# Kernel optimization log

Measured on AMD Instinct MI355X. Metric: run time of the kernel, lower is better.

Reference implementation:

```python
import jax, jax.numpy as jnp
import numpy as np

K = 16  # num neighbors


def setup_inputs() -> dict:
    key = jax.random.key(0)
    ks = jax.random.split(key, 10)
    B, N, d_in, d_out = 4, 8192, 64, 128
    h = d_out // 2
    return {
        "xyz": jax.random.normal(ks[0], (B, 3, N), jnp.float32),
        "feature": jax.random.normal(ks[1], (B, d_in, N), jnp.float32),
        "w1": jax.random.normal(ks[2], (h, 10), jnp.float32) * 0.1,
        "b1": jax.random.normal(ks[3], (h,), jnp.float32) * 0.1,
        "w2": jax.random.normal(ks[4], (h, h), jnp.float32) * 0.1,
        "b2": jax.random.normal(ks[5], (h,), jnp.float32) * 0.1,
        "w3": jax.random.normal(ks[6], (h, h), jnp.float32) * 0.1,
        "b3": jax.random.normal(ks[7], (h,), jnp.float32) * 0.1,
        "ws": jax.random.normal(ks[8], (d_out, d_in), jnp.float32) * 0.1,
        "bs": jax.random.normal(ks[9], (d_out,), jnp.float32) * 0.1,
    }


def reference(xyz, feature, w1, b1, w2, b2, w3, b3, ws, bs):
    # xyz: [B,3,N], feature: [B,d_in,N]
    xyz_t = jnp.transpose(xyz, (0, 2, 1))  # [B,N,3]
    sq = jnp.sum(xyz_t * xyz_t, axis=-1)  # [B,N]
    # squared pairwise distance [B,N,N]
    dist = sq[:, :, None] + sq[:, None, :] - 2.0 * jnp.einsum("bnc,bmc->bnm", xyz_t, xyz_t)
    _, idx = jax.lax.top_k(-dist, K)  # smallest-k -> [B,N,K]
    # gather neighbor coords: [B,N,K,3]
    knn_xyz = jax.vmap(lambda pts, ind: pts[ind])(xyz_t, idx)
    center = jnp.broadcast_to(xyz_t[:, :, None, :], knn_xyz.shape)  # [B,N,K,3]
    diff = knn_xyz - center
    dsq = jnp.sum(diff * diff, axis=-1, keepdims=True)  # [B,N,K,1]
    pos = jnp.concatenate([center, knn_xyz, diff, dsq], axis=-1)  # [B,N,K,10]
    # three 1x1 convs over channel dim (no activations, faithful to source)
    h = jnp.einsum("bnkc,oc->bnko", pos, w1) + b1
    h = jnp.einsum("bnkc,oc->bnko", h, w2) + b2
    h = jnp.einsum("bnkc,oc->bnko", h, w3) + b3
    fe = jnp.max(h, axis=2)  # max-pool over neighbors -> [B,N,d_out//2]
    fe = jnp.transpose(fe, (0, 2, 1))  # [B,d_out//2,N]
    shortcut = jnp.einsum("bcn,oc->bon", feature, ws) + bs[None, :, None]
    return jnp.concatenate([fe, fe], axis=1) + shortcut  # [B,d_out,N]
```

## Files before the change

### kernel.cpp

```cpp
#include <hip/hip_runtime.h>

#define B_ 4
#define N_ 8192
#define DIN 64
#define HDIM 64
#define DOUT 128
#define KNN 16
#define QPB 64
#define PART 8
#define NTHR (QPB * PART)
#define CHUNK (N_ / PART)
#define CAP 16
#define BLOCKS_PER_B (N_ / QPB)

__global__ __launch_bounds__(256) void k_prep(
    const float* __restrict__ xyz,
    const float* __restrict__ w1, const float* __restrict__ b1,
    const float* __restrict__ w2, const float* __restrict__ b2,
    const float* __restrict__ w3, const float* __restrict__ b3,
    float4* __restrict__ pk, float4* __restrict__ prm) {
  const int blk = blockIdx.x, t = threadIdx.x;
  const int b = blk >> 5;
  const int m = ((blk & 31) << 8) + t;
  const float* xb = xyz + (size_t)b * 3 * N_;
  float x = xb[m], y = xb[N_ + m], z = xb[2 * N_ + m];
  float sq = __fadd_rn(__fadd_rn(__fmul_rn(x, x), __fmul_rn(y, y)), __fmul_rn(z, z));
  pk[((size_t)b << 13) + m] = make_float4(x, y, z, sq);

  if (blk == 0) {
    __shared__ float M2[HDIM][10];
    __shared__ float bb[HDIM];
    const int o = t;
    if (o < HDIM) {
      float r[10];
#pragma unroll
      for (int c = 0; c < 10; c++) r[c] = 0.f;
      float s = b2[o];
      for (int l = 0; l < HDIM; l++) {
        float w = w2[o * HDIM + l];
#pragma unroll
        for (int c = 0; c < 10; c++) r[c] = fmaf(w, w1[l * 10 + c], r[c]);
        s = fmaf(w, b1[l], s);
      }
#pragma unroll
      for (int c = 0; c < 10; c++) M2[o][c] = r[c];
      bb[o] = s;
    }
    __syncthreads();
    if (o < HDIM) {
      float r3[10];
#pragma unroll
      for (int c = 0; c < 10; c++) r3[c] = 0.f;
      float bc = b3[o];
      for (int l = 0; l < HDIM; l++) {
        float w = w3[o * HDIM + l];
#pragma unroll
        for (int c = 0; c < 10; c++) r3[c] = fmaf(w, M2[l][c], r3[c]);
        bc = fmaf(w, bb[l], bc);
      }
      prm[o]      = make_float4(r3[0] - r3[6], r3[1] - r3[7], r3[2] - r3[8], bc);
      prm[64 + o] = make_float4(r3[3] + r3[6], r3[4] + r3[7], r3[5] + r3[8], r3[9]);
    }
  }
}

#define INSERT16(VARR, IARR, VMAX, DVAL, MIDX)                    \
  {                                                               \
    bool done = false;                                            \
    _Pragma("unroll") for (int _i = 0; _i < KNN; _i++) {          \
      bool hit = (!done) && (VARR[_i] == VMAX);                   \
      if (hit) { VARR[_i] = (DVAL); IARR[_i] = (MIDX); }          \
      done = done | hit;                                          \
    }                                                             \
    float _a = fmaxf(fmaxf(fmaxf(VARR[0], VARR[1]), fmaxf(VARR[2], VARR[3])),   \
                     fmaxf(fmaxf(VARR[4], VARR[5]), fmaxf(VARR[6], VARR[7])));  \
    float _b = fmaxf(fmaxf(fmaxf(VARR[8], VARR[9]), fmaxf(VARR[10], VARR[11])), \
                     fmaxf(fmaxf(VARR[12], VARR[13]), fmaxf(VARR[14], VARR[15])));\
    VMAX = fmaxf(_a, _b);                                         \
  }

#define MAX16(VARR, VMAX)                                         \
  {                                                               \
    float _a = fmaxf(fmaxf(fmaxf(VARR[0], VARR[1]), fmaxf(VARR[2], VARR[3])),   \
                     fmaxf(fmaxf(VARR[4], VARR[5]), fmaxf(VARR[6], VARR[7])));  \
    float _b = fmaxf(fmaxf(fmaxf(VARR[8], VARR[9]), fmaxf(VARR[10], VARR[11])), \
                     fmaxf(fmaxf(VARR[12], VARR[13]), fmaxf(VARR[14], VARR[15])));\
    VMAX = fmaxf(_a, _b);                                         \
  }

#define FLUSH()                                                   \
  {                                                               \
    for (int c_ = 0; c_ < cnt; c_++) {                            \
      float fd_ = poolF[c_ * NTHR + t];                           \
      int fm_ = poolI[c_ * NTHR + t];                             \
      if (fd_ < vmax) { INSERT16(v, id, vmax, fd_, fm_); }        \
    }                                                             \
    cnt = 0;                                                      \
    atomicMin(&tau[q], __float_as_uint(vmax));                    \
    gate = fminf(vmax, __uint_as_float(tau[q]));                  \
  }

__global__ __launch_bounds__(512, 4) void k_knn_fe(
    const float4* __restrict__ pk, const float4* __restrict__ prm,
    float* __restrict__ feBuf) {
  const int blk = blockIdx.x;
  const int b  = blk / BLOCKS_PER_B;
  const int n0 = (blk % BLOCKS_PER_B) * QPB;
  const int t = threadIdx.x;
  const int q = t & 63;
  const int j = __builtin_amdgcn_readfirstlane(t >> 6);

  __shared__ unsigned tau[QPB];
  __shared__ float4 prmL[2 * HDIM];
  __shared__ float poolF[CAP * NTHR];
  __shared__ unsigned short poolI[CAP * NTHR];

  if (t < QPB) tau[t] = 0x7f800000u;
  for (int i = t; i < 2 * HDIM; i += NTHR) prmL[i] = prm[i];

  const float4 qv = pk[((size_t)b << 13) + n0 + q];
  const float qx = qv.x, qy = qv.y, qz = qv.z, qs = qv.w;

  const float INF = __uint_as_float(0x7f800000u);
  float v[KNN]; int id[KNN];
#pragma unroll
  for (int i = 0; i < KNN; i++) { v[i] = INF; id[i] = 0; }
  float vmax = INF, gate = INF;
  int cnt = 0;
  __syncthreads();

  const float4* pj = pk + ((size_t)b << 13) + j * CHUNK;
  for (int u0 = 0; u0 < CHUNK; u0 += 8) {
    if (__any(cnt > CAP - 8)) { FLUSH(); }
    gate = fminf(gate, __uint_as_float(tau[q]));
    float4 c[8];
#pragma unroll
    for (int e = 0; e < 8; e++) c[e] = pj[u0 + e];
#pragma unroll
    for (int e = 0; e < 8; e++) {
      float dot = fmaf(c[e].z, qz, fmaf(c[e].y, qy, __fmul_rn(c[e].x, qx)));
      float d = __fsub_rn(__fadd_rn(qs, c[e].w), __fmul_rn(2.0f, dot));
      if (d < gate) {
        poolF[cnt * NTHR + t] = d;
        poolI[cnt * NTHR + t] = (unsigned short)(j * CHUNK + u0 + e);
        cnt++;
      }
    }
  }
  FLUSH();
  __syncthreads();

#pragma unroll
  for (int i = 0; i < KNN; i++) {
    poolF[(j * KNN + i) * QPB + q] = v[i];
    poolI[(j * KNN + i) * QPB + q] = (unsigned short)id[i];
  }
  __syncthreads();

  float fv[KNN]; int fid[KNN]; float fm = INF;
  if (j < 4) {
    const int r0 = (2 * j) * KNN, r1 = (2 * j + 1) * KNN;
#pragma unroll
    for (int i = 0; i < KNN; i++) {
      fv[i] = poolF[(r0 + i) * QPB + q];
      fid[i] = poolI[(r0 + i) * QPB + q];
    }
    MAX16(fv, fm);
    for (int s = 0; s < KNN; s++) {
      float d = poolF[(r1 + s) * QPB + q];
      if (d < fm) { int m_ = poolI[(r1 + s) * QPB + q]; INSERT16(fv, fid, fm, d, m_); }
    }
#pragma unroll
    for (int i = 0; i < KNN; i++) {
      poolF[(r0 + i) * QPB + q] = fv[i];
      poolI[(r0 + i) * QPB + q] = (unsigned short)fid[i];
    }
  }
  __syncthreads();

  if (j == 0) {
    for (int g = 1; g < 4; g++) {
      const int rg = (2 * g) * KNN;
      for (int s = 0; s < KNN; s++) {
        float d = poolF[(rg + s) * QPB + q];
        if (d < fm) { int m_ = poolI[(rg + s) * QPB + q]; INSERT16(fv, fid, fm, d, m_); }
      }
    }
#pragma unroll
    for (int i = 0; i < KNN; i++) poolI[i * QPB + q] = (unsigned short)fid[i];
  }
  __syncthreads();

#pragma unroll
  for (int kk = 0; kk < 2; kk++) {
    int k = j * 2 + kk;
    int m = poolI[k * QPB + q];
    float4 c = pk[((size_t)b << 13) + m];
    float dx = __fsub_rn(c.x, qx), dy = __fsub_rn(c.y, qy), dz = __fsub_rn(c.z, qz);
    float dsq = __fadd_rn(__fadd_rn(__fmul_rn(dx, dx), __fmul_rn(dy, dy)),
                          __fmul_rn(dz, dz));
    poolF[k * QPB + q] = c.x;
    poolF[(KNN + k) * QPB + q] = c.y;
    poolF[(2 * KNN + k) * QPB + q] = c.z;
    poolF[(3 * KNN + k) * QPB + q] = dsq;
  }
  __syncthreads();

  float nx[KNN], ny[KNN], nz[KNN], nd[KNN];
#pragma unroll
  for (int k = 0; k < KNN; k++) {
    nx[k] = poolF[k * QPB + q];
    ny[k] = poolF[(KNN + k) * QPB + q];
    nz[k] = poolF[(2 * KNN + k) * QPB + q];
    nd[k] = poolF[(3 * KNN + k) * QPB + q];
  }
  float fo[8];
#pragma unroll
  for (int oi = 0; oi < 8; oi++) {
    int o = j * 8 + oi;
    float4 pA = prmL[o], pB = prmL[HDIM + o];
    float basev = fmaf(qz, pA.z, fmaf(qy, pA.y, fmaf(qx, pA.x, pA.w)));
    float mx = -INF;
#pragma unroll
    for (int k = 0; k < KNN; k++) {
      float tv = fmaf(nz[k], pB.z,
                 fmaf(ny[k], pB.y,
                 fmaf(nx[k], pB.x, __fmul_rn(nd[k], pB.w))));
      mx = fmaxf(mx, tv);
    }
    fo[oi] = basev + mx;
  }
  float* feRow = feBuf + (size_t)(b * N_ + n0 + q) * HDIM + j * 8;
  ((float4*)feRow)[0] = make_float4(fo[0], fo[1], fo[2], fo[3]);
  ((float4*)feRow)[1] = make_float4(fo[4], fo[5], fo[6], fo[7]);
}

__global__ __launch_bounds__(256) void k_out(
    const float* __restrict__ feature, const float* __restrict__ wsM,
    const float* __restrict__ bs, const float* __restrict__ feBuf,
    float* __restrict__ out) {
  const int blk = blockIdx.x;
  const int b  = blk / BLOCKS_PER_B;
  const int n0 = (blk % BLOCKS_PER_B) * QPB;
  const int t = threadIdx.x;
  const int q = t & 63;
  const int jj = t >> 6;
  __shared__ float featL[DIN][QPB];
  __shared__ float wsL[DOUT][DIN];
#pragma unroll
  for (int r = 0; r < DIN; r += 4) {
    int c = r + jj;
    featL[c][q] = feature[(size_t)(b * DIN + c) * N_ + n0 + q];
  }
  for (int i = t; i < DOUT * DIN; i += 256) ((float*)wsL)[i] = wsM[i];
  __syncthreads();
  float f[DIN];
#pragma unroll
  for (int c = 0; c < DIN; c++) f[c] = featL[c][q];
  const float* feRow = feBuf + (size_t)(b * N_ + n0 + q) * HDIM;
  const int o0 = jj * 32;
  for (int oi = 0; oi < 32; oi++) {
    int o = o0 + oi;
    const float4* wr = (const float4*)wsL[o];
    float acc = 0.f;
#pragma unroll
    for (int c4 = 0; c4 < DIN / 4; c4++) {
      float4 w = wr[c4];
      acc = fmaf(w.x, f[4 * c4], acc);
      acc = fmaf(w.y, f[4 * c4 + 1], acc);
      acc = fmaf(w.z, f[4 * c4 + 2], acc);
      acc = fmaf(w.w, f[4 * c4 + 3], acc);
    }
    float r = acc + bs[o] + feRow[o & 63];
    out[(size_t)(b * DOUT + o) * N_ + n0 + q] = r;
  }
}

extern "C" void kernel_launch(void* const* d_in, const int* in_sizes, int n_in,
                              void* d_out, int out_size, void* d_ws, size_t ws_size,
                              hipStream_t stream) {
  const float* xyz     = (const float*)d_in[0];
  const float* feature = (const float*)d_in[1];
  const float* w1 = (const float*)d_in[2];
  const float* b1 = (const float*)d_in[3];
  const float* w2 = (const float*)d_in[4];
  const float* b2 = (const float*)d_in[5];
  const float* w3 = (const float*)d_in[6];
  const float* b3 = (const float*)d_in[7];
  const float* wsM = (const float*)d_in[8];
  const float* bs  = (const float*)d_in[9];
  float* out = (float*)d_out;

  float4* prm  = (float4*)d_ws;
  float4* pkB  = (float4*)((char*)d_ws + 8192);
  float* feBuf = (float*)((char*)d_ws + 8192 + (size_t)B_ * N_ * 16);

  hipLaunchKernelGGL(k_prep, dim3(128), dim3(256), 0, stream,
                     xyz, w1, b1, w2, b2, w3, b3, pkB, prm);
  hipLaunchKernelGGL(k_knn_fe, dim3(B_ * BLOCKS_PER_B), dim3(NTHR), 0, stream,
                     pkB, prm, feBuf);
  hipLaunchKernelGGL(k_out, dim3(B_ * BLOCKS_PER_B), dim3(256), 0, stream,
                     feature, wsM, bs, feBuf, out);
}
```

Measured before the change: 301.6 us.

## Fuse shortcut conv into KNN kernel, seed top-k from first points, tree-merge partials

Folds the output kernel (shortcut 1x1 conv plus the feature add) into the KNN kernel, reusing its shared-memory pools for the weights and features. This removes the intermediate feature buffer and one launch. The per-thread top-16 is now seeded with the first 16 real distances so the gate tightens right away. The final merge becomes a binary tree of 8 to 4 to 2 to 1 instead of a serial 3-way merge. The cost is that the tail GEMV work and the register pressure land inside a large, occupancy-limited kernel.

```diff
diff --git a/kernel.cpp b/kernel.cpp
--- a/kernel.cpp
+++ b/kernel.cpp
@@ -100,9 +100,10 @@
     gate = fminf(vmax, __uint_as_float(tau[q]));                  \
   }
 
-__global__ __launch_bounds__(512, 4) void k_knn_fe(
+__global__ __launch_bounds__(NTHR, 4) void k_knn_fe(
     const float4* __restrict__ pk, const float4* __restrict__ prm,
-    float* __restrict__ feBuf) {
+    const float* __restrict__ feature, const float* __restrict__ wsM,
+    const float* __restrict__ bs, float* __restrict__ out) {
   const int blk = blockIdx.x;
   const int b  = blk / BLOCKS_PER_B;
   const int n0 = (blk % BLOCKS_PER_B) * QPB;
@@ -112,8 +113,8 @@
 
   __shared__ unsigned tau[QPB];
   __shared__ float4 prmL[2 * HDIM];
-  __shared__ float poolF[CAP * NTHR];
-  __shared__ unsigned short poolI[CAP * NTHR];
+  __shared__ alignas(16) float poolF[CAP * NTHR];
+  __shared__ alignas(16) unsigned short poolI[CAP * NTHR];
 
   if (t < QPB) tau[t] = 0x7f800000u;
   for (int i = t; i < 2 * HDIM; i += NTHR) prmL[i] = prm[i];
@@ -123,14 +124,28 @@
 
   const float INF = __uint_as_float(0x7f800000u);
   float v[KNN]; int id[KNN];
-#pragma unroll
-  for (int i = 0; i < KNN; i++) { v[i] = INF; id[i] = 0; }
-  float vmax = INF, gate = INF;
+  float vmax, gate;
   int cnt = 0;
   __syncthreads();
 
   const float4* pj = pk + ((size_t)b << 13) + j * CHUNK;
-  for (int u0 = 0; u0 < CHUNK; u0 += 8) {
+
+  {
+    float4 c[KNN];
+#pragma unroll
+    for (int e = 0; e < KNN; e++) c[e] = pj[e];
+#pragma unroll
+    for (int e = 0; e < KNN; e++) {
+      float dot = fmaf(c[e].z, qz, fmaf(c[e].y, qy, __fmul_rn(c[e].x, qx)));
+      v[e] = __fsub_rn(__fadd_rn(qs, c[e].w), __fmul_rn(2.0f, dot));
+      id[e] = j * CHUNK + e;
+    }
+    MAX16(v, vmax);
+    atomicMin(&tau[q], __float_as_uint(vmax));
+    gate = fminf(vmax, __uint_as_float(tau[q]));
+  }
+
+  for (int u0 = KNN; u0 < CHUNK; u0 += 8) {
     if (__any(cnt > CAP - 8)) { FLUSH(); }
     gate = fminf(gate, __uint_as_float(tau[q]));
     float4 c[8];
@@ -159,11 +174,11 @@
 
   float fv[KNN]; int fid[KNN]; float fm = INF;
   if (j < 4) {
-    const int r0 = (2 * j) * KNN, r1 = (2 * j + 1) * KNN;
-#pragma unroll
-    for (int i = 0; i < KNN; i++) {
-      fv[i] = poolF[(r0 + i) * QPB + q];
-      fid[i] = poolI[(r0 + i) * QPB + q];
+    const int l0 = (2 * j) * KNN, r1 = (2 * j + 1) * KNN;
+#pragma unroll
+    for (int i = 0; i < KNN; i++) {
+      fv[i] = poolF[(l0 + i) * QPB + q];
+      fid[i] = poolI[(l0 + i) * QPB + q];
     }
     MAX16(fv, fm);
     for (int s = 0; s < KNN; s++) {
@@ -172,19 +187,40 @@
     }
 #pragma unroll
     for (int i = 0; i < KNN; i++) {
-      poolF[(r0 + i) * QPB + q] = fv[i];
-      poolI[(r0 + i) * QPB + q] = (unsigned short)fid[i];
-    }
-  }
-  __syncthreads();
-
+      poolF[(l0 + i) * QPB + q] = fv[i];
+      poolI[(l0 + i) * QPB + q] = (unsigned short)fid[i];
+    }
+  }
+  __syncthreads();
+  if (j < 2) {
+    const int l0 = (4 * j) * KNN, r1 = (4 * j + 2) * KNN;
+#pragma unroll
+    for (int i = 0; i < KNN; i++) {
+      fv[i] = poolF[(l0 + i) * QPB + q];
+      fid[i] = poolI[(l0 + i) * QPB + q];
+    }
+    MAX16(fv, fm);
+    for (int s = 0; s < KNN; s++) {
+      float d = poolF[(r1 + s) * QPB + q];
+      if (d < fm) { int m_ = poolI[(r1 + s) * QPB + q]; INSERT16(fv, fid, fm, d, m_); }
+    }
+#pragma unroll
+    for (int i = 0; i < KNN; i++) {
+      poolF[(l0 + i) * QPB + q] = fv[i];
+      poolI[(l0 + i) * QPB + q] = (unsigned short)fid[i];
+    }
+  }
+  __syncthreads();
   if (j == 0) {
-    for (int g = 1; g < 4; g++) {
-      const int rg = (2 * g) * KNN;
-      for (int s = 0; s < KNN; s++) {
-        float d = poolF[(rg + s) * QPB + q];
-        if (d < fm) { int m_ = poolI[(rg + s) * QPB + q]; INSERT16(fv, fid, fm, d, m_); }
-      }
+#pragma unroll
+    for (int i = 0; i < KNN; i++) {
+      fv[i] = poolF[i * QPB + q];
+      fid[i] = poolI[i * QPB + q];
+    }
+    MAX16(fv, fm);
+    for (int s = 0; s < KNN; s++) {
+      float d = poolF[(4 * KNN + s) * QPB + q];
+      if (d < fm) { int m_ = poolI[(4 * KNN + s) * QPB + q]; INSERT16(fv, fid, fm, d, m_); }
     }
 #pragma unroll
     for (int i = 0; i < KNN; i++) poolI[i * QPB + q] = (unsigned short)fid[i];
@@ -206,73 +242,67 @@
   }
   __syncthreads();
 
-  float nx[KNN], ny[KNN], nz[KNN], nd[KNN];
-#pragma unroll
-  for (int k = 0; k < KNN; k++) {
-    nx[k] = poolF[k * QPB + q];
-    ny[k] = poolF[(KNN + k) * QPB + q];
-    nz[k] = poolF[(2 * KNN + k) * QPB + q];
-    nd[k] = poolF[(3 * KNN + k) * QPB + q];
-  }
   float fo[8];
-#pragma unroll
-  for (int oi = 0; oi < 8; oi++) {
-    int o = j * 8 + oi;
-    float4 pA = prmL[o], pB = prmL[HDIM + o];
-    float basev = fmaf(qz, pA.z, fmaf(qy, pA.y, fmaf(qx, pA.x, pA.w)));
-    float mx = -INF;
+  {
+    float nx[KNN], ny[KNN], nz[KNN], nd[KNN];
 #pragma unroll
     for (int k = 0; k < KNN; k++) {
-      float tv = fmaf(nz[k], pB.z,
-                 fmaf(ny[k], pB.y,
-                 fmaf(nx[k], pB.x, __fmul_rn(nd[k], pB.w))));
-      mx = fmaxf(mx, tv);
-    }
-    fo[oi] = basev + mx;
-  }
-  float* feRow = feBuf + (size_t)(b * N_ + n0 + q) * HDIM + j * 8;
-  ((float4*)feRow)[0] = make_float4(fo[0], fo[1], fo[2], fo[3]);
-  ((float4*)feRow)[1] = make_float4(fo[4], fo[5], fo[6], fo[7]);
-}
-
-__global__ __launch_bounds__(256) void k_out(
-    const float* __restrict__ feature, const float* __restrict__ wsM,
-    const float* __restrict__ bs, const float* __restrict__ feBuf,
-    float* __restrict__ out) {
-  const int blk = blockIdx.x;
-  const int b  = blk / BLOCKS_PER_B;
-  const int n0 = (blk % BLOCKS_PER_B) * QPB;
-  const int t = threadIdx.x;
-  const int q = t & 63;
-  const int jj = t >> 6;
-  __shared__ float featL[DIN][QPB];
-  __shared__ float wsL[DOUT][DIN];
-#pragma unroll
-  for (int r = 0; r < DIN; r += 4) {
-    int c = r + jj;
-    featL[c][q] = feature[(size_t)(b * DIN + c) * N_ + n0 + q];
-  }
-  for (int i = t; i < DOUT * DIN; i += 256) ((float*)wsL)[i] = wsM[i];
-  __syncthreads();
-  float f[DIN];
-#pragma unroll
-  for (int c = 0; c < DIN; c++) f[c] = featL[c][q];
-  const float* feRow = feBuf + (size_t)(b * N_ + n0 + q) * HDIM;
-  const int o0 = jj * 32;
-  for (int oi = 0; oi < 32; oi++) {
-    int o = o0 + oi;
-    const float4* wr = (const float4*)wsL[o];
-    float acc = 0.f;
-#pragma unroll
-    for (int c4 = 0; c4 < DIN / 4; c4++) {
-      float4 w = wr[c4];
-      acc = fmaf(w.x, f[4 * c4], acc);
-      acc = fmaf(w.y, f[4 * c4 + 1], acc);
-      acc = fmaf(w.z, f[4 * c4 + 2], acc);
-      acc = fmaf(w.w, f[4 * c4 + 3], acc);
-    }
-    float r = acc + bs[o] + feRow[o & 63];
-    out[(size_t)(b * DOUT + o) * N_ + n0 + q] = r;
+      nx[k] = poolF[k * QPB + q];
+      ny[k] = poolF[(KNN + k) * QPB + q];
+      nz[k] = poolF[(2 * KNN + k) * QPB + q];
+      nd[k] = poolF[(3 * KNN + k) * QPB + q];
+    }
+#pragma unroll
+    for (int oi = 0; oi < 8; oi++) {
+      int o = j * 8 + oi;
+      float4 pA = prmL[o], pB = prmL[HDIM + o];
+      float basev = fmaf(qz, pA.z, fmaf(qy, pA.y, fmaf(qx, pA.x, pA.w)));
+      float mx = -INF;
+#pragma unroll
+      for (int k = 0; k < KNN; k++) {
+        float tv = fmaf(nz[k], pB.z,
+                   fmaf(ny[k], pB.y,
+                   fmaf(nx[k], pB.x, __fmul_rn(nd[k], pB.w))));
+        mx = fmaxf(mx, tv);
+      }
+      fo[oi] = basev + mx;
+    }
+  }
+  __syncthreads();
+
+  float* wsL = poolF;
+  float* feL = (float*)poolI;
+  for (int i = t; i < DOUT * DIN; i += NTHR) wsL[i] = wsM[i];
+#pragma unroll
+  for (int r = 0; r < 8; r++) {
+    int c = j * 8 + r;
+    feL[c * QPB + q] = feature[(size_t)(b * DIN + c) * N_ + n0 + q];
+  }
+  __syncthreads();
+
+  float acc[16];
+#pragma unroll
+  for (int oi = 0; oi < 16; oi++) acc[oi] = 0.f;
+  for (int c4 = 0; c4 < DIN / 4; c4++) {
+    float f0 = feL[(4 * c4 + 0) * QPB + q];
+    float f1 = feL[(4 * c4 + 1) * QPB + q];
+    float f2 = feL[(4 * c4 + 2) * QPB + q];
+    float f3 = feL[(4 * c4 + 3) * QPB + q];
+#pragma unroll
+    for (int oi = 0; oi < 16; oi++) {
+      int o = (oi < 8) ? (j * 8 + oi) : (64 + j * 8 + oi - 8);
+      float4 w = ((const float4*)(wsL + o * DIN))[c4];
+      acc[oi] = fmaf(w.x, f0, acc[oi]);
+      acc[oi] = fmaf(w.y, f1, acc[oi]);
+      acc[oi] = fmaf(w.z, f2, acc[oi]);
+      acc[oi] = fmaf(w.w, f3, acc[oi]);
+    }
+  }
+  float* ob = out + (size_t)b * DOUT * N_ + n0 + q;
+#pragma unroll
+  for (int oi = 0; oi < 16; oi++) {
+    int o = (oi < 8) ? (j * 8 + oi) : (64 + j * 8 + oi - 8);
+    ob[(size_t)o * N_] = acc[oi] + bs[o] + fo[oi & 7];
   }
 }
 
@@ -291,14 +321,11 @@
   const float* bs  = (const float*)d_in[9];
   float* out = (float*)d_out;
 
-  float4* prm  = (float4*)d_ws;
-  float4* pkB  = (float4*)((char*)d_ws + 8192);
-  float* feBuf = (float*)((char*)d_ws + 8192 + (size_t)B_ * N_ * 16);
+  float4* prm = (float4*)d_ws;
+  float4* pkB = (float4*)((char*)d_ws + 8192);
 
   hipLaunchKernelGGL(k_prep, dim3(128), dim3(256), 0, stream,
                      xyz, w1, b1, w2, b2, w3, b3, pkB, prm);
   hipLaunchKernelGGL(k_knn_fe, dim3(B_ * BLOCKS_PER_B), dim3(NTHR), 0, stream,
-                     pkB, prm, feBuf);
-  hipLaunchKernelGGL(k_out, dim3(B_ * BLOCKS_PER_B), dim3(256), 0, stream,
-                     feature, wsM, bs, feBuf, out);
+                     pkB, prm, feature, wsM, bs, out);
 }
```

Measured after the change: 286.4 us. 5.0% less time.
